# Optimization experiments

Measured on AMD Instinct MI355X. Metric: run time of the kernel, lower is better.

## Reference

```python
import jax, jax.numpy as jnp
import numpy as np

N_EMBED = 1024
HIDDEN = 2752  # find_multiple(int(8/3*1024), 32)
NUM_EXPERTS = 8
TOP_K = 2
AUX_COEFF = 0.01


def _swiglu(x, wg, wu, wd):
    # x: [N,C]; wg,wu: [H,C]; wd: [C,H]  (nn.Linear weight layout, y = x @ W.T)
    return (jax.nn.silu(x @ wg.T) * (x @ wu.T)) @ wd.T


def setup_inputs() -> dict:
    key = jax.random.key(0)
    ks = jax.random.split(key, 8)
    s = 0.02
    return {
        "x": jax.random.normal(ks[0], (2, 2048, N_EMBED), dtype=jnp.float32),
        "gate_w": jax.random.normal(ks[1], (NUM_EXPERTS, N_EMBED), dtype=jnp.float32) * s,
        "expert_gate_w": jax.random.normal(ks[2], (NUM_EXPERTS, HIDDEN, N_EMBED), dtype=jnp.float32) * s,
        "expert_up_w": jax.random.normal(ks[3], (NUM_EXPERTS, HIDDEN, N_EMBED), dtype=jnp.float32) * s,
        "expert_down_w": jax.random.normal(ks[4], (NUM_EXPERTS, N_EMBED, HIDDEN), dtype=jnp.float32) * s,
        "shared_gate_w": jax.random.normal(ks[5], (HIDDEN, N_EMBED), dtype=jnp.float32) * s,
        "shared_up_w": jax.random.normal(ks[6], (HIDDEN, N_EMBED), dtype=jnp.float32) * s,
        "shared_down_w": jax.random.normal(ks[7], (N_EMBED, HIDDEN), dtype=jnp.float32) * s,
    }


def reference(x, gate_w, expert_gate_w, expert_up_w, expert_down_w,
              shared_gate_w, shared_up_w, shared_down_w):
    B, T, C = x.shape
    xf = x.reshape(-1, C)                      # [N, C]
    N = xf.shape[0]

    # shared expert (always-on)
    shared_out = _swiglu(xf, shared_gate_w, shared_up_w, shared_down_w)

    # gating
    logits = xf @ gate_w.T                     # [N, E]
    top_w, top_i = jax.lax.top_k(logits, TOP_K)
    top_w = jax.nn.softmax(top_w.astype(jnp.float32), axis=-1)  # [N, K]

    # load-balancing aux loss
    mask = jax.nn.one_hot(top_i, NUM_EXPERTS, dtype=jnp.float32).sum(axis=1)  # [N, E]
    frac_selected = mask.mean(axis=0)
    mean_probs = jax.nn.softmax(logits.astype(jnp.float32), axis=-1).mean(axis=0)
    aux_loss = AUX_COEFF * (frac_selected * mean_probs).sum()

    # dense per-token per-expert combine weights (0 for unselected experts)
    w_dense = jnp.zeros((N, NUM_EXPERTS), jnp.float32)
    w_dense = w_dense.at[jnp.arange(N)[:, None], top_i].add(top_w)  # [N, E]

    routed = jnp.zeros_like(xf)
    for e in range(NUM_EXPERTS):
        routed = routed + _swiglu(xf, expert_gate_w[e], expert_up_w[e],
                                  expert_down_w[e]) * w_dense[:, e:e + 1]

    final = (shared_out + routed).reshape(B, T, C)
    return final, aux_loss
```

## Files before the change

kernel.cpp:

```cpp
#include <hip/hip_runtime.h>
#include <hip/hip_bf16.h>
#include <math.h>

#define N_TOK 4096
#define CDIM 1024
#define HDIM 2752
#define NEXP 8

typedef __bf16 bf16_t;
typedef __bf16 bf16x8 __attribute__((ext_vector_type(8)));
typedef float f32x4 __attribute__((ext_vector_type(4)));

__device__ __forceinline__ void gload_lds16(const void* g, void* l) {
  __builtin_amdgcn_global_load_lds(
      (const __attribute__((address_space(1))) unsigned int*)g,
      (__attribute__((address_space(3))) unsigned int*)l, 16, 0, 0);
}

__global__ void moe_cast(const float* __restrict__ in, bf16_t* __restrict__ outp) {
  size_t i = (size_t)blockIdx.x * 256 + threadIdx.x;
  float4 v = ((const float4*)in)[i];
  union { bf16_t b[4]; unsigned long long u; } pk;
  pk.b[0] = (bf16_t)v.x; pk.b[1] = (bf16_t)v.y; pk.b[2] = (bf16_t)v.z; pk.b[3] = (bf16_t)v.w;
  ((unsigned long long*)outp)[i] = pk.u;
}

__global__ void moe_gating(const float* __restrict__ x, const float* __restrict__ gw,
                           int* __restrict__ top_i, float* __restrict__ top_w,
                           float* __restrict__ probs_tok, bf16_t* __restrict__ xb) {
  const int wid = threadIdx.x >> 6, lane = threadIdx.x & 63;
  const int n = blockIdx.x * 4 + wid;
  const float* xr = x + (size_t)n * CDIM;
  float xv[16];
  for (int j = 0; j < 16; j += 4)
    *(float4*)&xv[j] = *(const float4*)(xr + lane * 16 + j);
  {
    union { bf16_t b[4]; unsigned long long u; } pk;
    unsigned long long* dst = (unsigned long long*)(xb + (size_t)n * CDIM + lane * 16);
    for (int j = 0; j < 16; j += 4) {
      pk.b[0] = (bf16_t)xv[j]; pk.b[1] = (bf16_t)xv[j+1];
      pk.b[2] = (bf16_t)xv[j+2]; pk.b[3] = (bf16_t)xv[j+3];
      dst[j >> 2] = pk.u;
    }
  }
  double part[NEXP];
  for (int e = 0; e < NEXP; ++e) {
    const float* gr = gw + e * CDIM + lane * 16;
    double s = 0.0;
    for (int j = 0; j < 16; j += 4) {
      float4 g = *(const float4*)(gr + j);
      s += (double)xv[j] * g.x + (double)xv[j+1] * g.y + (double)xv[j+2] * g.z + (double)xv[j+3] * g.w;
    }
    part[e] = s;
  }
  for (int off = 32; off; off >>= 1)
    for (int e = 0; e < NEXP; ++e) part[e] += __shfl_xor(part[e], off);
  if (lane == 0) {
    int i0 = 0; double l0 = part[0];
    for (int e = 1; e < NEXP; ++e) if (part[e] > l0) { l0 = part[e]; i0 = e; }
    int i1 = -1; double l1 = -1e300;
    for (int e = 0; e < NEXP; ++e) if (e != i0 && part[e] > l1) { l1 = part[e]; i1 = e; }
    double ed = exp(l1 - l0);
    float w0 = (float)(1.0 / (1.0 + ed));
    float w1 = (float)(ed / (1.0 + ed));
    top_i[2*n] = i0; top_i[2*n+1] = i1;
    top_w[2*n] = w0; top_w[2*n+1] = w1;
    double Z = 0.0, pe[NEXP];
    for (int e = 0; e < NEXP; ++e) { pe[e] = exp(part[e] - l0); Z += pe[e]; }
    for (int e = 0; e < NEXP; ++e) probs_tok[(size_t)n * NEXP + e] = (float)(pe[e] / Z);
  }
}

__global__ void moe_reduce(const float* __restrict__ probs_tok, const int* __restrict__ top_i,
                           int* __restrict__ cnts, float* __restrict__ probs_sum) {
  const int e = blockIdx.x, t = threadIdx.x;
  float s = 0.f; int c = 0;
  for (int n = t; n < N_TOK; n += 256) {
    s += probs_tok[(size_t)n * NEXP + e];
    c += (top_i[2*n] == e) + (top_i[2*n+1] == e);
  }
  __shared__ float ls[256]; __shared__ int lc[256];
  ls[t] = s; lc[t] = c; __syncthreads();
  for (int o = 128; o; o >>= 1) {
    if (t < o) { ls[t] += ls[t+o]; lc[t] += lc[t+o]; }
    __syncthreads();
  }
  if (t == 0) { cnts[e] = lc[0]; probs_sum[e] = ls[0]; }
}

__global__ void moe_prefix_aux(const int* __restrict__ cnts, int* __restrict__ offs,
                               int* __restrict__ cursors, const float* __restrict__ probs_sum,
                               float* __restrict__ out_aux) {
  if (threadIdx.x == 0) {
    int o = 0;
    for (int e = 0; e < NEXP; ++e) { offs[e] = o; o += cnts[e]; }
    double aux = 0.0;
    for (int e = 0; e < NEXP; ++e) aux += (double)cnts[e] * (double)probs_sum[e];
    out_aux[0] = (float)(0.01 * aux / ((double)N_TOK * (double)N_TOK));
  }
  if (threadIdx.x < NEXP) cursors[threadIdx.x] = 0;
}

__global__ void moe_scatter(const int* __restrict__ top_i, const float* __restrict__ top_w,
                            const int* __restrict__ offs, int* __restrict__ cursors,
                            int* __restrict__ rowlist, float* __restrict__ wlist,
                            int* __restrict__ pair_pos) {
  const int wid = threadIdx.x >> 6, lane = threadIdx.x & 63;
  const int n = (blockIdx.x * 4 + wid) * 64 + lane;
  const unsigned long long lt = ((unsigned long long)1 << lane) - 1;
  const int e0 = top_i[2*n], e1 = top_i[2*n + 1];
  const float w0 = top_w[2*n], w1 = top_w[2*n + 1];
  for (int e = 0; e < NEXP; ++e) {
    unsigned long long m0 = __ballot(e0 == e);
    unsigned long long m1 = __ballot(e1 == e);
    int tot = __popcll(m0) + __popcll(m1);
    int base = 0;
    if (lane == 0 && tot) base = atomicAdd(&cursors[e], tot);
    base = __shfl(base, 0);
    if (e0 == e) {
      int p = offs[e] + base + __popcll(m0 & lt);
      rowlist[p] = n; wlist[p] = w0; pair_pos[2*n] = p;
    }
    if (e1 == e) {
      int p = offs[e] + base + __popcll(m0) + __popcll(m1 & lt);
      rowlist[p] = n; wlist[p] = w1; pair_pos[2*n + 1] = p;
    }
  }
}

__launch_bounds__(256)
__global__ void moe_gu(const bf16_t* __restrict__ xb,
                       const bf16_t* __restrict__ Wg_r, const bf16_t* __restrict__ Wu_r,
                       const bf16_t* __restrict__ Wg_s, const bf16_t* __restrict__ Wu_s,
                       bf16_t* __restrict__ hout,
                       const int* __restrict__ rowlist, const int* __restrict__ offs,
                       const int* __restrict__ cnts) {
  const int z = blockIdx.z;
  const bool routed = z < NEXP;
  int cnt, hbase, loff = 0;
  const bf16_t *Wg, *Wu;
  if (routed) {
    cnt = cnts[z]; loff = offs[z]; hbase = loff;
    if ((int)blockIdx.y * 128 >= cnt) return;
    Wg = Wg_r + (size_t)z * HDIM * CDIM;
    Wu = Wu_r + (size_t)z * HDIM * CDIM;
  } else {
    cnt = N_TOK; hbase = 2 * N_TOK;
    Wg = Wg_s; Wu = Wu_s;
  }
  const int m0 = blockIdx.y * 128, n0 = blockIdx.x * 64;

  __shared__ alignas(16) bf16_t lA[128 * 64];
  __shared__ alignas(16) bf16_t lB[128 * 64];

  const int tid = threadIdx.x, wid = tid >> 6, lane = tid & 63;
  const int r8 = lane >> 3, c8 = lane & 7;
  const int fr = lane & 15, hi = lane >> 4;

  const bf16_t* gA[4];
  for (int i = 0; i < 4; ++i) {
    int r = wid * 32 + i * 8 + r8;
    int tok;
    if (routed) { int mm = m0 + r < cnt ? m0 + r : cnt - 1; tok = rowlist[loff + mm]; }
    else tok = m0 + r;
    gA[i] = xb + (size_t)tok * CDIM + c8 * 8;
  }
  const bf16_t* gB[4];
  for (int i = 0; i < 4; ++i) {
    int br = wid * 32 + i * 8 + r8;
    gB[i] = (br < 64 ? Wg + (size_t)(n0 + br) * CDIM
                     : Wu + (size_t)(n0 + br - 64) * CDIM) + c8 * 8;
  }

  f32x4 accG[2][4] = {}; f32x4 accU[2][4] = {};

  for (int kt = 0; kt < CDIM / 64; ++kt) {
    if (kt) __syncthreads();
    for (int i = 0; i < 4; ++i) gload_lds16(gA[i] + kt * 64, lA + (wid * 32 + i * 8) * 64);
    for (int i = 0; i < 4; ++i) gload_lds16(gB[i] + kt * 64, lB + (wid * 32 + i * 8) * 64);
    __syncthreads();
    for (int kk = 0; kk < 2; ++kk) {
      const int kb = kk * 32 + hi * 8;
      bf16x8 a[2], bg[4], bu[4];
      for (int i = 0; i < 2; ++i) a[i] = *(const bf16x8*)(lA + (wid * 32 + i * 16 + fr) * 64 + kb);
      for (int j = 0; j < 4; ++j) {
        bg[j] = *(const bf16x8*)(lB + (j * 16 + fr) * 64 + kb);
        bu[j] = *(const bf16x8*)(lB + (64 + j * 16 + fr) * 64 + kb);
      }
      for (int i = 0; i < 2; ++i)
        for (int j = 0; j < 4; ++j) {
          accG[i][j] = __builtin_amdgcn_mfma_f32_16x16x32_bf16(a[i], bg[j], accG[i][j], 0, 0, 0);
          accU[i][j] = __builtin_amdgcn_mfma_f32_16x16x32_bf16(a[i], bu[j], accU[i][j], 0, 0, 0);
        }
    }
  }
  for (int i = 0; i < 2; ++i)
    for (int j = 0; j < 4; ++j)
      for (int r = 0; r < 4; ++r) {
        int lm = wid * 32 + i * 16 + hi * 4 + r;
        if (routed && m0 + lm >= cnt) continue;
        float g = accG[i][j][r], u = accU[i][j][r];
        float hv = (g / (1.f + __expf(-g))) * u;
        hout[(size_t)(hbase + m0 + lm) * HDIM + n0 + j * 16 + fr] = (bf16_t)hv;
      }
}

__launch_bounds__(256)
__global__ void moe_down(const bf16_t* __restrict__ hin, const bf16_t* __restrict__ Wd_r,
                         const bf16_t* __restrict__ Wd_s,
                         float* __restrict__ outp, float* __restrict__ eo,
                         const float* __restrict__ wlist,
                         const int* __restrict__ offs, const int* __restrict__ cnts) {
  const int z = blockIdx.z;
  const bool routed = z < NEXP;
  int cnt, hbase;
  const bf16_t* Wd;
  if (routed) {
    cnt = cnts[z]; hbase = offs[z];
    if ((int)blockIdx.y * 128 >= cnt) return;
    Wd = Wd_r + (size_t)z * CDIM * HDIM;
  } else {
    cnt = N_TOK; hbase = 2 * N_TOK;
    Wd = Wd_s;
  }
  const int m0 = blockIdx.y * 128, n0 = blockIdx.x * 128;

  __shared__ alignas(16) bf16_t lA[128 * 64];
  __shared__ alignas(16) bf16_t lB[128 * 64];

  const int tid = threadIdx.x, wid = tid >> 6, lane = tid & 63;
  const int wm = wid >> 1, wn = wid & 1;
  const int r8 = lane >> 3, c8 = lane & 7;
  const int fr = lane & 15, hi = lane >> 4;

  const bf16_t* gA[4];
  for (int i = 0; i < 4; ++i) {
    int r = wid * 32 + i * 8 + r8;
    int mm = (routed && m0 + r >= cnt) ? cnt - 1 : m0 + r;
    gA[i] = hin + (size_t)(hbase + mm) * HDIM + c8 * 8;
  }
  const bf16_t* gB[4];
  for (int i = 0; i < 4; ++i) {
    int br = wid * 32 + i * 8 + r8;
    gB[i] = Wd + (size_t)(n0 + br) * HDIM + c8 * 8;
  }

  f32x4 acc[4][4] = {};

  for (int kt = 0; kt < HDIM / 64; ++kt) {
    if (kt) __syncthreads();
    for (int i = 0; i < 4; ++i) gload_lds16(gA[i] + kt * 64, lA + (wid * 32 + i * 8) * 64);
    for (int i = 0; i < 4; ++i) gload_lds16(gB[i] + kt * 64, lB + (wid * 32 + i * 8) * 64);
    __syncthreads();
    for (int kk = 0; kk < 2; ++kk) {
      const int kb = kk * 32 + hi * 8;
      bf16x8 a[4], b[4];
      for (int i = 0; i < 4; ++i) a[i] = *(const bf16x8*)(lA + (wm * 64 + i * 16 + fr) * 64 + kb);
      for (int j = 0; j < 4; ++j) b[j] = *(const bf16x8*)(lB + (wn * 64 + j * 16 + fr) * 64 + kb);
      for (int i = 0; i < 4; ++i)
        for (int j = 0; j < 4; ++j)
          acc[i][j] = __builtin_amdgcn_mfma_f32_16x16x32_bf16(a[i], b[j], acc[i][j], 0, 0, 0);
    }
  }
  for (int i = 0; i < 4; ++i)
    for (int j = 0; j < 4; ++j)
      for (int r = 0; r < 4; ++r) {
        int lm = wm * 64 + i * 16 + hi * 4 + r;
        if (routed && m0 + lm >= cnt) continue;
        float v = acc[i][j][r];
        int col = n0 + wn * 64 + j * 16 + fr;
        if (routed) {
          int pos = hbase + m0 + lm;
          eo[(size_t)pos * CDIM + col] = v * wlist[pos];
        } else {
          outp[(size_t)(m0 + lm) * CDIM + col] = v;
        }
      }
}

__global__ void moe_combine(float* __restrict__ outp, const float* __restrict__ eo,
                            const int* __restrict__ pair_pos) {
  size_t i4 = (size_t)blockIdx.x * 256 + threadIdx.x;
  int n = (int)(i4 >> 8);
  int c4 = (int)(i4 & 255);
  int p0 = pair_pos[2*n], p1 = pair_pos[2*n + 1];
  const float4* eo4 = (const float4*)eo;
  float4 a = ((const float4*)outp)[i4];
  float4 b = eo4[(size_t)p0 * 256 + c4];
  float4 c = eo4[(size_t)p1 * 256 + c4];
  float4 r;
  r.x = a.x + b.x + c.x; r.y = a.y + b.y + c.y;
  r.z = a.z + b.z + c.z; r.w = a.w + b.w + c.w;
  ((float4*)outp)[i4] = r;
}

extern "C" void kernel_launch(void* const* d_in, const int* in_sizes, int n_in,
                              void* d_out, int out_size, void* d_ws, size_t ws_size,
                              hipStream_t stream) {
  const float* x   = (const float*)d_in[0];
  const float* gw  = (const float*)d_in[1];
  const float* egw = (const float*)d_in[2];
  const float* euw = (const float*)d_in[3];
  const float* edw = (const float*)d_in[4];
  const float* sgw = (const float*)d_in[5];
  const float* suw = (const float*)d_in[6];
  const float* sdw = (const float*)d_in[7];
  float* out = (float*)d_out;

  char* ws = (char*)d_ws;
  size_t off = 0;
  auto alloc = [&](size_t bytes) -> void* {
    void* p = ws + off; off = (off + bytes + 255) & ~(size_t)255; return p;
  };
  const size_t EW = (size_t)NEXP * HDIM * CDIM;
  const size_t SW = (size_t)HDIM * CDIM;
  bf16_t* xb    = (bf16_t*)alloc((size_t)N_TOK * CDIM * 2);
  bf16_t* egw_b = (bf16_t*)alloc(EW * 2);
  bf16_t* euw_b = (bf16_t*)alloc(EW * 2);
  bf16_t* edw_b = (bf16_t*)alloc(EW * 2);
  bf16_t* sgw_b = (bf16_t*)alloc(SW * 2);
  bf16_t* suw_b = (bf16_t*)alloc(SW * 2);
  bf16_t* sdw_b = (bf16_t*)alloc(SW * 2);
  bf16_t* h     = (bf16_t*)alloc((size_t)(3 * N_TOK + 256) * HDIM * 2);
  float*  eo    = (float*)alloc((size_t)2 * N_TOK * CDIM * 4);
  int*    ctrl  = (int*)alloc(256);
  int* cnts = ctrl; int* cursors = ctrl + 8; int* offs = ctrl + 16;
  float* probs_sum = (float*)(ctrl + 24);
  int*   top_i    = (int*)alloc((size_t)N_TOK * 2 * 4);
  float* top_w    = (float*)alloc((size_t)N_TOK * 2 * 4);
  int*   pair_pos = (int*)alloc((size_t)N_TOK * 2 * 4);
  int*   rowlist  = (int*)alloc((size_t)2 * N_TOK * 4);
  float* wlist    = (float*)alloc((size_t)2 * N_TOK * 4);
  float* probs_tok = (float*)alloc((size_t)N_TOK * NEXP * 4);

  moe_cast<<<(int)(EW / 1024), 256, 0, stream>>>(egw, egw_b);
  moe_cast<<<(int)(EW / 1024), 256, 0, stream>>>(euw, euw_b);
  moe_cast<<<(int)(EW / 1024), 256, 0, stream>>>(edw, edw_b);
  moe_cast<<<(int)(SW / 1024), 256, 0, stream>>>(sgw, sgw_b);
  moe_cast<<<(int)(SW / 1024), 256, 0, stream>>>(suw, suw_b);
  moe_cast<<<(int)(SW / 1024), 256, 0, stream>>>(sdw, sdw_b);

  moe_gating<<<1024, 256, 0, stream>>>(x, gw, top_i, top_w, probs_tok, xb);
  moe_reduce<<<NEXP, 256, 0, stream>>>(probs_tok, top_i, cnts, probs_sum);
  moe_prefix_aux<<<1, 64, 0, stream>>>(cnts, offs, cursors, probs_sum, out + (size_t)N_TOK * CDIM);
  moe_scatter<<<16, 256, 0, stream>>>(top_i, top_w, offs, cursors, rowlist, wlist, pair_pos);

  moe_gu<<<dim3(HDIM / 64, N_TOK / 128, NEXP + 1), 256, 0, stream>>>(
      xb, egw_b, euw_b, sgw_b, suw_b, h, rowlist, offs, cnts);
  moe_down<<<dim3(CDIM / 128, N_TOK / 128, NEXP + 1), 256, 0, stream>>>(
      h, edw_b, sdw_b, out, eo, wlist, offs, cnts);
  moe_combine<<<4096, 256, 0, stream>>>(out, eo, pair_pos);
}
```

Measured before the change: 499.2 us.

## Fuse expert combine into down-projection via atomic adds and merge weight casts

The down-projection kernel now scatters weighted expert outputs directly into the zeroed output with float atomicAdd, indexed through rowlist. This removes the eo intermediate buffer, the pair_pos bookkeeping and the separate combine kernel. The six weight cast launches are also merged into a single launch that uses a block-range table. The atomics add contention and make the floating-point summation order nondeterministic, and the output now needs a memset first.

Measured after the change: 483.3 us. 3.2% less time.

```diff
diff --git a/kernel.cpp b/kernel.cpp
--- a/kernel.cpp
+++ b/kernel.cpp
@@ -17,12 +17,22 @@
       (__attribute__((address_space(3))) unsigned int*)l, 16, 0, 0);
 }
 
-__global__ void moe_cast(const float* __restrict__ in, bf16_t* __restrict__ outp) {
-  size_t i = (size_t)blockIdx.x * 256 + threadIdx.x;
-  float4 v = ((const float4*)in)[i];
-  union { bf16_t b[4]; unsigned long long u; } pk;
-  pk.b[0] = (bf16_t)v.x; pk.b[1] = (bf16_t)v.y; pk.b[2] = (bf16_t)v.z; pk.b[3] = (bf16_t)v.w;
-  ((unsigned long long*)outp)[i] = pk.u;
+struct Cast6 {
+  const float* src[6];
+  bf16_t* dst[6];
+  int start[7];
+};
+__global__ void moe_cast6(Cast6 c) {
+  int b = blockIdx.x;
+  int k = 0;
+#pragma unroll
+  for (int i = 0; i < 5; ++i) k += (b >= c.start[i + 1]);
+  size_t i4 = (size_t)(b - c.start[k]) * 256 + threadIdx.x;
+  float4 v = ((const float4*)c.src[k])[i4];
+  union { bf16_t b4[4]; unsigned long long u; } pk;
+  pk.b4[0] = (bf16_t)v.x; pk.b4[1] = (bf16_t)v.y;
+  pk.b4[2] = (bf16_t)v.z; pk.b4[3] = (bf16_t)v.w;
+  ((unsigned long long*)c.dst[k])[i4] = pk.u;
 }
 
 __global__ void moe_gating(const float* __restrict__ x, const float* __restrict__ gw,
@@ -103,8 +113,7 @@
 
 __global__ void moe_scatter(const int* __restrict__ top_i, const float* __restrict__ top_w,
                             const int* __restrict__ offs, int* __restrict__ cursors,
-                            int* __restrict__ rowlist, float* __restrict__ wlist,
-                            int* __restrict__ pair_pos) {
+                            int* __restrict__ rowlist, float* __restrict__ wlist) {
   const int wid = threadIdx.x >> 6, lane = threadIdx.x & 63;
   const int n = (blockIdx.x * 4 + wid) * 64 + lane;
   const unsigned long long lt = ((unsigned long long)1 << lane) - 1;
@@ -119,11 +128,11 @@
     base = __shfl(base, 0);
     if (e0 == e) {
       int p = offs[e] + base + __popcll(m0 & lt);
-      rowlist[p] = n; wlist[p] = w0; pair_pos[2*n] = p;
+      rowlist[p] = n; wlist[p] = w0;
     }
     if (e1 == e) {
       int p = offs[e] + base + __popcll(m0) + __popcll(m1 & lt);
-      rowlist[p] = n; wlist[p] = w1; pair_pos[2*n + 1] = p;
+      rowlist[p] = n; wlist[p] = w1;
     }
   }
 }
@@ -208,8 +217,8 @@
 __launch_bounds__(256)
 __global__ void moe_down(const bf16_t* __restrict__ hin, const bf16_t* __restrict__ Wd_r,
                          const bf16_t* __restrict__ Wd_s,
-                         float* __restrict__ outp, float* __restrict__ eo,
-                         const float* __restrict__ wlist,
+                         float* __restrict__ outp,
+                         const float* __restrict__ wlist, const int* __restrict__ rowlist,
                          const int* __restrict__ offs, const int* __restrict__ cnts) {
   const int z = blockIdx.z;
   const bool routed = z < NEXP;
@@ -271,27 +280,12 @@
         int col = n0 + wn * 64 + j * 16 + fr;
         if (routed) {
           int pos = hbase + m0 + lm;
-          eo[(size_t)pos * CDIM + col] = v * wlist[pos];
+          int tok = rowlist[pos];
+          atomicAdd(&outp[(size_t)tok * CDIM + col], v * wlist[pos]);
         } else {
-          outp[(size_t)(m0 + lm) * CDIM + col] = v;
+          atomicAdd(&outp[(size_t)(m0 + lm) * CDIM + col], v);
         }
       }
-}
-
-__global__ void moe_combine(float* __restrict__ outp, const float* __restrict__ eo,
-                            const int* __restrict__ pair_pos) {
-  size_t i4 = (size_t)blockIdx.x * 256 + threadIdx.x;
-  int n = (int)(i4 >> 8);
-  int c4 = (int)(i4 & 255);
-  int p0 = pair_pos[2*n], p1 = pair_pos[2*n + 1];
-  const float4* eo4 = (const float4*)eo;
-  float4 a = ((const float4*)outp)[i4];
-  float4 b = eo4[(size_t)p0 * 256 + c4];
-  float4 c = eo4[(size_t)p1 * 256 + c4];
-  float4 r;
-  r.x = a.x + b.x + c.x; r.y = a.y + b.y + c.y;
-  r.z = a.z + b.z + c.z; r.w = a.w + b.w + c.w;
-  ((float4*)outp)[i4] = r;
 }
 
 extern "C" void kernel_launch(void* const* d_in, const int* in_sizes, int n_in,
@@ -322,32 +316,39 @@
   bf16_t* suw_b = (bf16_t*)alloc(SW * 2);
   bf16_t* sdw_b = (bf16_t*)alloc(SW * 2);
   bf16_t* h     = (bf16_t*)alloc((size_t)(3 * N_TOK + 256) * HDIM * 2);
-  float*  eo    = (float*)alloc((size_t)2 * N_TOK * CDIM * 4);
   int*    ctrl  = (int*)alloc(256);
   int* cnts = ctrl; int* cursors = ctrl + 8; int* offs = ctrl + 16;
   float* probs_sum = (float*)(ctrl + 24);
   int*   top_i    = (int*)alloc((size_t)N_TOK * 2 * 4);
   float* top_w    = (float*)alloc((size_t)N_TOK * 2 * 4);
-  int*   pair_pos = (int*)alloc((size_t)N_TOK * 2 * 4);
   int*   rowlist  = (int*)alloc((size_t)2 * N_TOK * 4);
   float* wlist    = (float*)alloc((size_t)2 * N_TOK * 4);
   float* probs_tok = (float*)alloc((size_t)N_TOK * NEXP * 4);
 
-  moe_cast<<<(int)(EW / 1024), 256, 0, stream>>>(egw, egw_b);
-  moe_cast<<<(int)(EW / 1024), 256, 0, stream>>>(euw, euw_b);
-  moe_cast<<<(int)(EW / 1024), 256, 0, stream>>>(edw, edw_b);
-  moe_cast<<<(int)(SW / 1024), 256, 0, stream>>>(sgw, sgw_b);
-  moe_cast<<<(int)(SW / 1024), 256, 0, stream>>>(suw, suw_b);
-  moe_cast<<<(int)(SW / 1024), 256, 0, stream>>>(sdw, sdw_b);
+  hipMemsetAsync(out, 0, (size_t)N_TOK * CDIM * 4, stream);
+
+  Cast6 c6;
+  c6.src[0] = egw; c6.dst[0] = egw_b;
+  c6.src[1] = euw; c6.dst[1] = euw_b;
+  c6.src[2] = edw; c6.dst[2] = edw_b;
+  c6.src[3] = sgw; c6.dst[3] = sgw_b;
+  c6.src[4] = suw; c6.dst[4] = suw_b;
+  c6.src[5] = sdw; c6.dst[5] = sdw_b;
+  int ew_blk = (int)(EW / 1024), sw_blk = (int)(SW / 1024);
+  c6.start[0] = 0;
+  c6.start[1] = ew_blk;     c6.start[2] = 2 * ew_blk; c6.start[3] = 3 * ew_blk;
+  c6.start[4] = 3 * ew_blk + sw_blk;
+  c6.start[5] = 3 * ew_blk + 2 * sw_blk;
+  c6.start[6] = 3 * ew_blk + 3 * sw_blk;
+  moe_cast6<<<c6.start[6], 256, 0, stream>>>(c6);
 
   moe_gating<<<1024, 256, 0, stream>>>(x, gw, top_i, top_w, probs_tok, xb);
   moe_reduce<<<NEXP, 256, 0, stream>>>(probs_tok, top_i, cnts, probs_sum);
   moe_prefix_aux<<<1, 64, 0, stream>>>(cnts, offs, cursors, probs_sum, out + (size_t)N_TOK * CDIM);
-  moe_scatter<<<16, 256, 0, stream>>>(top_i, top_w, offs, cursors, rowlist, wlist, pair_pos);
+  moe_scatter<<<16, 256, 0, stream>>>(top_i, top_w, offs, cursors, rowlist, wlist);
 
   moe_gu<<<dim3(HDIM / 64, N_TOK / 128, NEXP + 1), 256, 0, stream>>>(
       xb, egw_b, euw_b, sgw_b, suw_b, h, rowlist, offs, cnts);
   moe_down<<<dim3(CDIM / 128, N_TOK / 128, NEXP + 1), 256, 0, stream>>>(
-      h, edw_b, sdw_b, out, eo, wlist, offs, cnts);
-  moe_combine<<<4096, 256, 0, stream>>>(out, eo, pair_pos);
-}
+      h, edw_b, sdw_b, out, wlist, rowlist, offs, cnts);
+}
```
